# Kernel optimization log

Hardware: AMD Instinct MI355X
Metric: run time of the kernel (lower is better)

## Reference

```python
import jax, jax.numpy as jnp
import numpy as np
import math

D = 4096            # input dim and all hidden dims
TOKENS = (4, 2048)  # batch, seq
P = 0.8             # excitatory fraction for EI layers


def conn_dense(kernel, x):
    # bool kernel interpreted as +1 (True) / -1 (False)
    w = jnp.where(kernel, jnp.asarray(1.0, x.dtype), jnp.asarray(-1.0, x.dtype))
    return x @ w


def ei_dense(x, kernel, scale, p):
    in_dim = x.shape[-1]
    ne = round(in_dim * p)  # excitatory count
    x_exc = x[..., :ne]
    x_inh = x[..., ne:]
    xx = jnp.concatenate([x_exc, (-p / (1.0 - p)) * x_inh], axis=-1)
    return scale * conn_dense(kernel, xx)


def setup_inputs() -> dict:
    key = jax.random.key(0)
    ks = jax.random.split(key, 4)
    x = jax.random.normal(ks[0], (*TOKENS, D), dtype=jnp.float32)
    k0 = jax.random.bernoulli(ks[1], 0.5, (D, D))
    k1 = jax.random.bernoulli(ks[2], 0.5, (D, D))
    k2 = jax.random.bernoulli(ks[3], 0.5, (D, D))
    s = jnp.asarray(1.0 / math.sqrt(D), dtype=jnp.float32)
    return {"x": x, "k0": k0, "s0": s, "k1": k1, "s1": s, "k2": k2, "s2": s}


def reference(x, k0, s0, k1, s1, k2, s2):
    # layer 0: Dense_01 (plain +/-1 matmul, scale), then relu*2
    h = s0 * conn_dense(k0, x)
    h = jax.nn.relu(h) * 2.0
    # layer 1: Dense_EI, then relu*2
    h = ei_dense(h, k1, s1, P)
    h = jax.nn.relu(h) * 2.0
    # layer 2: Dense_EI (no activation on last layer)
    return ei_dense(h, k2, s2, P)
```

## Files before the change

kernel.cpp:

```cpp
#include <hip/hip_runtime.h>
#include <stdint.h>

#define DD 4096
#define NE_IDX 3277

typedef __attribute__((ext_vector_type(8))) short short8;
typedef __attribute__((ext_vector_type(16))) float f32x16;
typedef __attribute__((ext_vector_type(4))) unsigned int u32x4;

__device__ __forceinline__ unsigned short f2bf(float f) {
    unsigned int u = __float_as_uint(f);
    u += 0x7fffu + ((u >> 16) & 1u);
    return (unsigned short)(u >> 16);
}

__device__ __forceinline__ void gload16(const void* g, void* l) {
    __builtin_amdgcn_global_load_lds(
        (const __attribute__((address_space(1))) unsigned int*)g,
        (__attribute__((address_space(3))) unsigned int*)l,
        16, 0, 0);
}

__global__ void detect_kernel(const unsigned int* __restrict__ k0, int* __restrict__ flag) {
    if (blockIdx.x == 0 && threadIdx.x == 0) {
        int ok4 = 1;
        for (int i = 0; i < 256; ++i) {
            unsigned int v = k0[i];
            if (!(v == 0u || v == 1u || v == 0x3f800000u)) { ok4 = 0; break; }
        }
        *flag = ok4;
    }
}

__global__ void pack_x_kernel(const float* __restrict__ x, unsigned short* __restrict__ xb, int n8) {
    const int stride = gridDim.x * blockDim.x;
    for (int i = blockIdx.x * blockDim.x + threadIdx.x; i < n8; i += stride) {
        const float4* p = (const float4*)(x + (size_t)i * 8);
        float4 a = p[0], b = p[1];
        short8 r;
        r[0] = (short)f2bf(a.x); r[1] = (short)f2bf(a.y);
        r[2] = (short)f2bf(a.z); r[3] = (short)f2bf(a.w);
        r[4] = (short)f2bf(b.x); r[5] = (short)f2bf(b.y);
        r[6] = (short)f2bf(b.z); r[7] = (short)f2bf(b.w);
        *(short8*)(xb + (size_t)i * 8) = r;
    }
}

__global__ void pack_w_kernel(const void* __restrict__ kin, unsigned short* __restrict__ wt,
                              const float* __restrict__ sptr, float inh, int ne,
                              const int* __restrict__ flag) {
    __shared__ unsigned short tile[64][68];
    const int elem4 = *flag;
    const float s = *sptr;
    const int i0 = blockIdx.x * 64;
    const int j0 = blockIdx.y * 64;
    const int t = threadIdx.x;
    {
        const int il = t >> 2;
        const int jc = (t & 3) * 16;
        const int gi = i0 + il;
        const float mag = s * ((gi < ne) ? 1.0f : inh);
        const unsigned short pos = f2bf(mag);
        const unsigned short neg = f2bf(-mag);
        if (elem4) {
            const unsigned int* k32 = (const unsigned int*)kin + (size_t)gi * DD + j0 + jc;
            #pragma unroll
            for (int q = 0; q < 4; ++q) {
                u32x4 v = *(const u32x4*)(k32 + q * 4);
                #pragma unroll
                for (int e = 0; e < 4; ++e)
                    tile[il][jc + q * 4 + e] = v[e] ? pos : neg;
            }
        } else {
            const unsigned char* k8 = (const unsigned char*)kin + (size_t)gi * DD + j0 + jc;
            u32x4 v = *(const u32x4*)k8;
            #pragma unroll
            for (int q = 0; q < 4; ++q) {
                unsigned int w = v[q];
                tile[il][jc + q * 4 + 0] = (w & 0xffu) ? pos : neg;
                tile[il][jc + q * 4 + 1] = ((w >> 8) & 0xffu) ? pos : neg;
                tile[il][jc + q * 4 + 2] = ((w >> 16) & 0xffu) ? pos : neg;
                tile[il][jc + q * 4 + 3] = ((w >> 24) & 0xffu) ? pos : neg;
            }
        }
    }
    __syncthreads();
    {
        const int jl = t >> 2;
        const int ic = (t & 3) * 16;
        short8 o0, o1;
        #pragma unroll
        for (int e = 0; e < 8; ++e) o0[e] = (short)tile[ic + e][jl];
        #pragma unroll
        for (int e = 0; e < 8; ++e) o1[e] = (short)tile[ic + 8 + e][jl];
        unsigned short* dst = wt + (size_t)(j0 + jl) * DD + i0 + ic;
        *(short8*)(dst) = o0;
        *(short8*)(dst + 8) = o1;
    }
}

#define PH32(MH, NH, LA, LB, STAGE_STMT, EB) do {                               \
    if (LA) {                                                                   \
        _Pragma("unroll")                                                       \
        for (int mi = 0; mi < 2; ++mi)                                          \
            _Pragma("unroll")                                                   \
            for (int s = 0; s < 4; ++s)                                         \
                af[mi][s] = *(const short8*)(Lc + (ab2[(MH)*2+mi] ^ (s<<5)));   \
    }                                                                           \
    if (LB) {                                                                   \
        _Pragma("unroll")                                                       \
        for (int s = 0; s < 4; ++s)                                             \
            bf[(NH)][s] = *(const short8*)(Lc + (bb2[(NH)] ^ (s<<5)));          \
    }                                                                           \
    STAGE_STMT;                                                                 \
    asm volatile("s_waitcnt vmcnt(4)" ::: "memory");                            \
    __builtin_amdgcn_s_barrier();                                               \
    asm volatile("s_waitcnt lgkmcnt(0)" ::: "memory");                          \
    __builtin_amdgcn_sched_barrier(0);                                          \
    __builtin_amdgcn_s_setprio(1);                                              \
    _Pragma("unroll")                                                           \
    for (int s = 0; s < 4; ++s)                                                 \
        _Pragma("unroll")                                                       \
        for (int mi = 0; mi < 2; ++mi)                                          \
            acc[(MH)*2+mi][(NH)] = __builtin_amdgcn_mfma_f32_32x32x16_bf16(     \
                af[mi][s], bf[(NH)][s], acc[(MH)*2+mi][(NH)], 0, 0, 0);         \
    __builtin_amdgcn_s_setprio(0);                                              \
    __builtin_amdgcn_sched_barrier(0);                                          \
    if (EB) __builtin_amdgcn_s_barrier();                                       \
} while (0)

template <int MODE>
__global__ __launch_bounds__(512, 2)
void gemm256_kernel(const unsigned short* __restrict__ A,
                    const unsigned short* __restrict__ Bt,
                    void* __restrict__ Cout)
{
    __shared__ unsigned short L[65536];
    const char* Lc = (const char*)L;

    const int tid  = threadIdx.x;
    const int lane = tid & 63;
    const int l31  = lane & 31;
    const int hb   = lane >> 5;
    const int wave = tid >> 6;
    const int wr   = wave >> 2;
    const int wc   = wave & 3;

    int wg = blockIdx.x;
    const int per = gridDim.x >> 3;
    wg = (wg & 7) * per + (wg >> 3);
    const int tm = wg >> 4;
    const int tn = wg & 15;

    const size_t arow0 = (size_t)tm * 256;
    const size_t brow0 = (size_t)tn * 256;

    const int sx  = (tid & 15) ^ ((tid >> 4) & 15);
    const int kcS = (sx & 7) << 3;
    const int rbS = sx >> 3;
    const int arowloc = ((tid >> 4) << 1) + rbS;
    const int lcl = tid & 255;
    const int seg = tid >> 8;
    const int browloc = ((lcl >> 4) << 1) + rbS;

    auto stageA = [&](int sb, int c, int kt) {
        #pragma unroll
        for (int q = 0; q < 2; ++q) {
            gload16(A + ((arow0 + c * 64 + q * 128 + arowloc) << 12) + kt + kcS,
                    (void*)&L[sb + (c * 32 + q * 64) * 128 + tid * 8]);
        }
    };
    auto stageB = [&](int sb, int c, int kt) {
        #pragma unroll
        for (int q = 0; q < 2; ++q) {
            const int d0 = c * 16 + seg * 32 + q * 64;
            gload16(Bt + ((brow0 + d0 * 2 + browloc) << 12) + kt + kcS,
                    (void*)&L[sb + 16384 + d0 * 128 + lcl * 8]);
        }
    };

    const int slot0 = (hb | ((l31 & 1) << 3)) ^ (l31 >> 1);
    int ab2[4], bb2[2];
    #pragma unroll
    for (int mt = 0; mt < 4; ++mt) {
        const int d = wr * 64 + mt * 16 + (l31 >> 1);
        ab2[mt] = (d << 8) + (slot0 << 4);
    }
    #pragma unroll
    for (int nt = 0; nt < 2; ++nt) {
        const int d = wc * 32 + nt * 16 + (l31 >> 1);
        bb2[nt] = 32768 + (d << 8) + (slot0 << 4);
    }

    short8 af[2][4], bf[2][4];
    f32x16 acc[4][2];
    #pragma unroll
    for (int m = 0; m < 4; ++m)
        #pragma unroll
        for (int n = 0; n < 2; ++n)
            #pragma unroll
            for (int e = 0; e < 16; ++e)
                acc[m][n][e] = 0.f;

    stageA(0, 0, 0); stageB(0, 0, 0); stageB(0, 1, 0); stageA(0, 1, 0);
    asm volatile("s_waitcnt vmcnt(4)" ::: "memory");
    __builtin_amdgcn_s_barrier();
    __builtin_amdgcn_sched_barrier(0);

    for (int t = 0; t < 63; ++t) {
        const int sb  = ((t & 1) ^ 1) * 32768;
        const int kt1 = (t + 1) * 64;
        PH32(0, 0, 1, 1, stageA(sb, 0, kt1), 0);
        PH32(0, 1, 0, 1, stageB(sb, 0, kt1), 0);
        PH32(1, 1, 1, 0, stageB(sb, 1, kt1), 0);
        PH32(1, 0, 0, 0, stageA(sb, 1, kt1), 1);
        #pragma unroll
        for (int i = 0; i < 4; ++i) ab2[i] ^= 65536;
        bb2[0] ^= 65536; bb2[1] ^= 65536;
    }
    asm volatile("s_waitcnt vmcnt(0)" ::: "memory");
    __builtin_amdgcn_s_barrier();
    __builtin_amdgcn_sched_barrier(0);
    PH32(0, 0, 1, 1, (void)0, 0);
    PH32(0, 1, 0, 1, (void)0, 0);
    PH32(1, 1, 1, 0, (void)0, 0);
    PH32(1, 0, 0, 0, (void)0, 0);

    const int orow0 = tm * 256 + wr * 128 + hb * 4;
    const int ocol0 = tn * 256 + wc * 64 + l31;
    #pragma unroll
    for (int mt = 0; mt < 4; ++mt) {
        #pragma unroll
        for (int nt = 0; nt < 2; ++nt) {
            #pragma unroll
            for (int reg = 0; reg < 16; ++reg) {
                const int row = orow0 + mt * 32 + (reg & 3) + 8 * (reg >> 2);
                const int col = ocol0 + nt * 32;
                float v = acc[mt][nt][reg];
                if (MODE == 1) {
                    v = fmaxf(v, 0.0f) * 2.0f;
                    ((unsigned short*)Cout)[((size_t)row << 12) + col] = f2bf(v);
                } else {
                    ((float*)Cout)[((size_t)row << 12) + col] = v;
                }
            }
        }
    }
}

extern "C" void kernel_launch(void* const* d_in, const int* in_sizes, int n_in,
                              void* d_out, int out_size, void* d_ws, size_t ws_size,
                              hipStream_t stream) {
    const float* x  = (const float*)d_in[0];
    const void*  k0 = d_in[1];
    const float* s0 = (const float*)d_in[2];
    const void*  k1 = d_in[3];
    const float* s1 = (const float*)d_in[4];
    const void*  k2 = d_in[5];
    const float* s2 = (const float*)d_in[6];

    const int M = in_sizes[0] / DD;

    const size_t act_bytes = (size_t)M * DD * 2;
    const size_t w_bytes   = (size_t)DD * DD * 2;
    const size_t need      = act_bytes * 2 + w_bytes + 256;
    if (ws_size < need) return;

    char* ws = (char*)d_ws;
    unsigned short* xb = (unsigned short*)ws;
    unsigned short* h1 = (unsigned short*)(ws + act_bytes);
    unsigned short* wt = (unsigned short*)(ws + act_bytes * 2);
    int* flag          = (int*)(ws + act_bytes * 2 + w_bytes);

    detect_kernel<<<1, 64, 0, stream>>>((const unsigned int*)k0, flag);
    pack_x_kernel<<<2048, 256, 0, stream>>>(x, xb, M * DD / 8);

    dim3 pw_grid(DD / 64, DD / 64);
    const int gemm_grid = (M / 256) * (DD / 256);

    pack_w_kernel<<<pw_grid, 256, 0, stream>>>(k0, wt, s0, 1.0f, DD, flag);
    gemm256_kernel<1><<<gemm_grid, 512, 0, stream>>>(xb, wt, h1);

    pack_w_kernel<<<pw_grid, 256, 0, stream>>>(k1, wt, s1, -4.0f, NE_IDX, flag);
    gemm256_kernel<1><<<gemm_grid, 512, 0, stream>>>(h1, wt, xb);

    pack_w_kernel<<<pw_grid, 256, 0, stream>>>(k2, wt, s2, -4.0f, NE_IDX, flag);
    gemm256_kernel<0><<<gemm_grid, 512, 0, stream>>>(xb, wt, (float*)d_out);
}
```

Before: 733.5 us.

## Deepen GEMM global-to-LDS prefetch to stage sub-tiles two k-steps ahead

Restructures the 256x256 bf16 MFMA GEMM main loop so most A/B sub-tile loads for k-step t+2 are issued into the buffer just consumed. The prologue and epilogue are rewritten to match. The vmcnt wait moves from before each phase's barrier to once per iteration after the last phase, and every phase now ends with a barrier. The aim is more latency hiding for global loads. In exchange it adds barriers per phase and carries a risk of LDS buffer hazards from the overlapped staging order.

```diff
diff --git a/kernel.cpp b/kernel.cpp
--- a/kernel.cpp
+++ b/kernel.cpp
@@ -99,7 +99,7 @@
     }
 }
 
-#define PH32(MH, NH, LA, LB, STAGE_STMT, EB) do {                               \
+#define PH32(MH, NH, LA, LB, STAGE_STMT, VM) do {                               \
     if (LA) {                                                                   \
         _Pragma("unroll")                                                       \
         for (int mi = 0; mi < 2; ++mi)                                          \
@@ -113,7 +113,6 @@
             bf[(NH)][s] = *(const short8*)(Lc + (bb2[(NH)] ^ (s<<5)));          \
     }                                                                           \
     STAGE_STMT;                                                                 \
-    asm volatile("s_waitcnt vmcnt(4)" ::: "memory");                            \
     __builtin_amdgcn_s_barrier();                                               \
     asm volatile("s_waitcnt lgkmcnt(0)" ::: "memory");                          \
     __builtin_amdgcn_sched_barrier(0);                                          \
@@ -126,7 +125,9 @@
                 af[mi][s], bf[(NH)][s], acc[(MH)*2+mi][(NH)], 0, 0, 0);         \
     __builtin_amdgcn_s_setprio(0);                                              \
     __builtin_amdgcn_sched_barrier(0);                                          \
-    if (EB) __builtin_amdgcn_s_barrier();                                       \
+    if ((VM) == 1) asm volatile("s_waitcnt vmcnt(4)" ::: "memory");             \
+    if ((VM) == 2) asm volatile("s_waitcnt vmcnt(0)" ::: "memory");             \
+    __builtin_amdgcn_s_barrier();                                               \
 } while (0)
 
 template <int MODE>
@@ -202,25 +203,32 @@
             for (int e = 0; e < 16; ++e)
                 acc[m][n][e] = 0.f;
 
-    stageA(0, 0, 0); stageB(0, 0, 0); stageB(0, 1, 0); stageA(0, 1, 0);
+    stageA(0, 0, 0); stageA(0, 1, 0); stageB(0, 0, 0); stageB(0, 1, 0);
+    stageB(32768, 0, 64); stageB(32768, 1, 64); stageA(32768, 0, 64);
     asm volatile("s_waitcnt vmcnt(4)" ::: "memory");
     __builtin_amdgcn_s_barrier();
     __builtin_amdgcn_sched_barrier(0);
 
-    for (int t = 0; t < 63; ++t) {
-        const int sb  = ((t & 1) ^ 1) * 32768;
+    for (int t = 0; t < 62; ++t) {
+        const int sbn = ((t & 1) ^ 1) * 32768;
+        const int sbc = (t & 1) * 32768;
         const int kt1 = (t + 1) * 64;
-        PH32(0, 0, 1, 1, stageA(sb, 0, kt1), 0);
-        PH32(0, 1, 0, 1, stageB(sb, 0, kt1), 0);
-        PH32(1, 1, 1, 0, stageB(sb, 1, kt1), 0);
-        PH32(1, 0, 0, 0, stageA(sb, 1, kt1), 1);
+        const int kt2 = (t + 2) * 64;
+        PH32(0, 0, 1, 1, stageA(sbn, 1, kt1), 0);
+        PH32(0, 1, 0, 1, stageB(sbc, 0, kt2), 0);
+        PH32(1, 1, 1, 0, stageB(sbc, 1, kt2), 0);
+        PH32(1, 0, 0, 0, stageA(sbc, 0, kt2), 1);
         #pragma unroll
         for (int i = 0; i < 4; ++i) ab2[i] ^= 65536;
         bb2[0] ^= 65536; bb2[1] ^= 65536;
     }
-    asm volatile("s_waitcnt vmcnt(0)" ::: "memory");
-    __builtin_amdgcn_s_barrier();
-    __builtin_amdgcn_sched_barrier(0);
+    PH32(0, 0, 1, 1, stageA(32768, 1, 63 * 64), 0);
+    PH32(0, 1, 0, 1, (void)0, 0);
+    PH32(1, 1, 1, 0, (void)0, 0);
+    PH32(1, 0, 0, 0, (void)0, 2);
+    #pragma unroll
+    for (int i = 0; i < 4; ++i) ab2[i] ^= 65536;
+    bb2[0] ^= 65536; bb2[1] ^= 65536;
     PH32(0, 0, 1, 1, (void)0, 0);
     PH32(0, 1, 0, 1, (void)0, 0);
     PH32(1, 1, 1, 0, (void)0, 0);
```

After: 760.6 us. 1.04x slower.

## Software-pipeline LDS fragment reads ahead of MFMA phases in GEMM main loop

Applied to the files above, without the earlier changes.

Restructures the GEMM inner loop so LDS reads for the next A/B fragment halves are issued before the current MFMA block runs, using double-buffered A fragments in registers. Each phase's fragments come from the previous phase's reads, so LDS latency overlaps with matrix math, and one barrier per iteration is dropped. In exchange the kernel holds more fragment registers, which may press occupancy at 2 blocks of 512 threads, and the barrier and waitcnt ordering across the LDS double buffer becomes harder to get right.

```diff
diff --git a/kernel.cpp b/kernel.cpp
--- a/kernel.cpp
+++ b/kernel.cpp
@@ -20,6 +20,13 @@
         (__attribute__((address_space(3))) unsigned int*)l,
         16, 0, 0);
 }
+
+#define VMC4 asm volatile("s_waitcnt vmcnt(4)" ::: "memory")
+#define VMC2 asm volatile("s_waitcnt vmcnt(2)" ::: "memory")
+#define VMC0 asm volatile("s_waitcnt vmcnt(0)" ::: "memory")
+#define LGKM do { asm volatile("s_waitcnt lgkmcnt(0)" ::: "memory"); \
+                  __builtin_amdgcn_sched_barrier(0); } while (0)
+#define BAR  __builtin_amdgcn_s_barrier()
 
 __global__ void detect_kernel(const unsigned int* __restrict__ k0, int* __restrict__ flag) {
     if (blockIdx.x == 0 && threadIdx.x == 0) {
@@ -99,36 +106,6 @@
     }
 }
 
-#define PH32(MH, NH, LA, LB, STAGE_STMT, EB) do {                               \
-    if (LA) {                                                                   \
-        _Pragma("unroll")                                                       \
-        for (int mi = 0; mi < 2; ++mi)                                          \
-            _Pragma("unroll")                                                   \
-            for (int s = 0; s < 4; ++s)                                         \
-                af[mi][s] = *(const short8*)(Lc + (ab2[(MH)*2+mi] ^ (s<<5)));   \
-    }                                                                           \
-    if (LB) {                                                                   \
-        _Pragma("unroll")                                                       \
-        for (int s = 0; s < 4; ++s)                                             \
-            bf[(NH)][s] = *(const short8*)(Lc + (bb2[(NH)] ^ (s<<5)));          \
-    }                                                                           \
-    STAGE_STMT;                                                                 \
-    asm volatile("s_waitcnt vmcnt(4)" ::: "memory");                            \
-    __builtin_amdgcn_s_barrier();                                               \
-    asm volatile("s_waitcnt lgkmcnt(0)" ::: "memory");                          \
-    __builtin_amdgcn_sched_barrier(0);                                          \
-    __builtin_amdgcn_s_setprio(1);                                              \
-    _Pragma("unroll")                                                           \
-    for (int s = 0; s < 4; ++s)                                                 \
-        _Pragma("unroll")                                                       \
-        for (int mi = 0; mi < 2; ++mi)                                          \
-            acc[(MH)*2+mi][(NH)] = __builtin_amdgcn_mfma_f32_32x32x16_bf16(     \
-                af[mi][s], bf[(NH)][s], acc[(MH)*2+mi][(NH)], 0, 0, 0);         \
-    __builtin_amdgcn_s_setprio(0);                                              \
-    __builtin_amdgcn_sched_barrier(0);                                          \
-    if (EB) __builtin_amdgcn_s_barrier();                                       \
-} while (0)
-
 template <int MODE>
 __global__ __launch_bounds__(512, 2)
 void gemm256_kernel(const unsigned short* __restrict__ A,
@@ -180,19 +157,11 @@
     };
 
     const int slot0 = (hb | ((l31 & 1) << 3)) ^ (l31 >> 1);
-    int ab2[4], bb2[2];
-    #pragma unroll
-    for (int mt = 0; mt < 4; ++mt) {
-        const int d = wr * 64 + mt * 16 + (l31 >> 1);
-        ab2[mt] = (d << 8) + (slot0 << 4);
-    }
-    #pragma unroll
-    for (int nt = 0; nt < 2; ++nt) {
-        const int d = wc * 32 + nt * 16 + (l31 >> 1);
-        bb2[nt] = 32768 + (d << 8) + (slot0 << 4);
-    }
-
-    short8 af[2][4], bf[2][4];
+    int abase = ((wr * 64 + (l31 >> 1)) << 8) + (slot0 << 4);
+    int bbase = 32768 + ((wc * 32 + (l31 >> 1)) << 8) + (slot0 << 4);
+
+    short8 af[2][2][4];
+    short8 bf[2][4];
     f32x16 acc[4][2];
     #pragma unroll
     for (int m = 0; m < 4; ++m)
@@ -202,29 +171,54 @@
             for (int e = 0; e < 16; ++e)
                 acc[m][n][e] = 0.f;
 
+    auto RD_A = [&](int h) {
+        #pragma unroll
+        for (int s = 0; s < 4; ++s)
+            #pragma unroll
+            for (int mi = 0; mi < 2; ++mi)
+                af[h][mi][s] = *(const short8*)(Lc + (abase ^ (s << 5)) + ((h * 2 + mi) << 12));
+    };
+    auto RD_B = [&](int h) {
+        #pragma unroll
+        for (int s = 0; s < 4; ++s)
+            bf[h][s] = *(const short8*)(Lc + (bbase ^ (s << 5)) + (h << 12));
+    };
+    auto MM = [&](int ah, int bh) {
+        __builtin_amdgcn_s_setprio(1);
+        #pragma unroll
+        for (int s = 0; s < 4; ++s)
+            #pragma unroll
+            for (int mi = 0; mi < 2; ++mi)
+                acc[ah * 2 + mi][bh] = __builtin_amdgcn_mfma_f32_32x32x16_bf16(
+                    af[ah][mi][s], bf[bh][s], acc[ah * 2 + mi][bh], 0, 0, 0);
+        __builtin_amdgcn_s_setprio(0);
+        __builtin_amdgcn_sched_barrier(0);
+    };
+
     stageA(0, 0, 0); stageB(0, 0, 0); stageB(0, 1, 0); stageA(0, 1, 0);
-    asm volatile("s_waitcnt vmcnt(4)" ::: "memory");
-    __builtin_amdgcn_s_barrier();
+    VMC4; BAR;
     __builtin_amdgcn_sched_barrier(0);
+    RD_A(0); RD_B(0);
 
     for (int t = 0; t < 63; ++t) {
-        const int sb  = ((t & 1) ^ 1) * 32768;
-        const int kt1 = (t + 1) * 64;
-        PH32(0, 0, 1, 1, stageA(sb, 0, kt1), 0);
-        PH32(0, 1, 0, 1, stageB(sb, 0, kt1), 0);
-        PH32(1, 1, 1, 0, stageB(sb, 1, kt1), 0);
-        PH32(1, 0, 0, 0, stageA(sb, 1, kt1), 1);
-        #pragma unroll
-        for (int i = 0; i < 4; ++i) ab2[i] ^= 65536;
-        bb2[0] ^= 65536; bb2[1] ^= 65536;
-    }
-    asm volatile("s_waitcnt vmcnt(0)" ::: "memory");
-    __builtin_amdgcn_s_barrier();
-    __builtin_amdgcn_sched_barrier(0);
-    PH32(0, 0, 1, 1, (void)0, 0);
-    PH32(0, 1, 0, 1, (void)0, 0);
-    PH32(1, 1, 1, 0, (void)0, 0);
-    PH32(1, 0, 0, 0, (void)0, 0);
+        const int sb  = ((t + 1) & 1) * 32768;
+        const int kt2 = (t + 1) * 64;
+        stageA(sb, 0, kt2); VMC4; BAR; LGKM;
+        RD_B(1); MM(0, 0);
+        stageB(sb, 0, kt2); VMC4; BAR; LGKM;
+        RD_A(1); MM(0, 1);
+        stageB(sb, 1, kt2); LGKM;
+        MM(1, 0);
+        stageA(sb, 1, kt2); VMC4; BAR; LGKM;
+        abase ^= 65536; bbase ^= 65536;
+        RD_A(0); RD_B(0); MM(1, 1);
+    }
+    VMC2; BAR; LGKM;
+    RD_B(1); MM(0, 0);
+    VMC0; BAR; LGKM;
+    RD_A(1); MM(0, 1);
+    LGKM; MM(1, 0);
+    LGKM; MM(1, 1);
 
     const int orow0 = tm * 256 + wr * 128 + hb * 4;
     const int ocol0 = tn * 256 + wc * 64 + l31;
```

Result: no change. 729.6 us (-0.5%).
